# Kernel optimization log

Hardware: AMD Instinct MI355X
Metric: run time of the kernel (lower is better)

## Reference

```python
import jax, jax.numpy as jnp
import numpy as np

N = 65536      # occupied voxels
D = 96         # voxel grid extent per axis
CIN = 64
CH = 64
COUT = 16      # 8 * 2
K = 27         # 3^3 kernel offsets


def _build_neighbor_idx(rng):
    # unique occupied voxel coordinates
    lin = rng.choice(D ** 3, size=N, replace=False).astype(np.int64)
    coords = np.stack(np.unravel_index(lin, (D, D, D)), axis=1)  # [N,3]
    grid = np.full(D ** 3, -1, dtype=np.int32)
    grid[lin] = np.arange(N, dtype=np.int32)
    # 27 offsets in {-1,0,1}^3 (MinkowskiEngine kernel map, stride 1)
    offs = np.stack(np.meshgrid(*([np.arange(-1, 2)] * 3), indexing='ij'),
                    axis=-1).reshape(K, 3)
    nc = coords[:, None, :] + offs[None, :, :]            # [N,27,3]
    valid = np.all((nc >= 0) & (nc < D), axis=-1)         # [N,27]
    nlin = (nc[..., 0] * D + nc[..., 1]) * D + nc[..., 2]
    nidx = np.where(valid, grid[np.clip(nlin, 0, D ** 3 - 1)], -1)
    return nidx.astype(np.int32)                          # -1 = no neighbor


def setup_inputs() -> dict:
    key = jax.random.key(0)
    ks = jax.random.split(key, 7)
    rng = np.random.default_rng(0)
    neighbor_idx = jnp.asarray(_build_neighbor_idx(rng))
    s1 = 1.0 / np.sqrt(K * CIN)
    s2 = 1.0 / np.sqrt(K * CH)
    return {
        'x': jax.random.normal(ks[0], (N, CIN), jnp.float32),
        'neighbor_idx': neighbor_idx,
        'W1': jax.random.normal(ks[1], (K, CIN, CH), jnp.float32) * s1,
        'b1': jax.random.normal(ks[2], (CH,), jnp.float32) * 0.1,
        'W2': jax.random.normal(ks[3], (K, CH, CH), jnp.float32) * s2,
        'b2': jax.random.normal(ks[4], (CH,), jnp.float32) * 0.1,
        'W3': jax.random.normal(ks[5], (K, CH, COUT), jnp.float32) * s2,
        'b3': jax.random.normal(ks[6], (COUT,), jnp.float32) * 0.1,
    }


def _sparse_conv(feat, W, b, nidx):
    # feat: [N,Cin], W: [K,Cin,Cout], nidx: [N,K] with -1 for missing
    mask = nidx >= 0
    gathered = jnp.where(mask[..., None],
                         feat[jnp.clip(nidx, 0)], 0.0)    # [N,K,Cin]
    return jnp.einsum('nkc,kcd->nd', gathered, W) + b


def reference(x, neighbor_idx, W1, b1, W2, b2, W3, b3):
    h = jax.nn.relu(_sparse_conv(x, W1, b1, neighbor_idx))
    h = jax.nn.relu(_sparse_conv(h, W2, b2, neighbor_idx))
    return _sparse_conv(h, W3, b3, neighbor_idx)
```

## Files before the change

### kernel.cpp

```cpp
#include <hip/hip_runtime.h>
#include <hip/hip_bf16.h>
#include <stdint.h>

#define N_VOX 65536
#define NK 27
#define BR 64

typedef float f32x4  __attribute__((ext_vector_type(4)));
typedef float f32x16 __attribute__((ext_vector_type(16)));
typedef int   i32x2  __attribute__((ext_vector_type(2)));
typedef __bf16 bf16x8 __attribute__((ext_vector_type(8)));

#define WAITVM(n) asm volatile("s_waitcnt vmcnt(" #n ")" ::: "memory")

__device__ __forceinline__ void barrier_fence() {
    asm volatile("" ::: "memory");
    __builtin_amdgcn_s_barrier();
    asm volatile("" ::: "memory");
}

__device__ __forceinline__ void gll16(const void* src, uint32_t lds_addr) {
    asm volatile("s_mov_b32 m0, %0\n\t"
                 "global_load_lds_dwordx4 %1, off"
                 :: "s"(lds_addr), "v"(src)
                 : "memory");
}

__device__ __forceinline__ void wconv_elem(const float* __restrict__ W,
                                           __bf16* __restrict__ Wt, int Dc, int i) {
    int d = i % Dc;
    int c = (i / Dc) % 64;
    int k = i / (Dc * 64);
    int off = ((d * 128 + ((c >> 3) << 4)) ^ ((d & 7) << 4)) + (c & 7) * 2;
    *(__bf16*)((char*)Wt + (size_t)k * Dc * 128 + off) = (__bf16)W[i];
}

#define PREP_CVT   2048
#define PREP_W1    432
#define PREP_W2    432
#define PREP_W3    108
#define PREP_GRID  (PREP_CVT + PREP_W1 + PREP_W2 + PREP_W3 + 1)
__global__ __launch_bounds__(256) void prep_kernel(
    const float* __restrict__ x,
    const float* __restrict__ W1, const float* __restrict__ W2, const float* __restrict__ W3,
    __bf16* __restrict__ xb, __bf16* __restrict__ Wt1, __bf16* __restrict__ Wt2,
    __bf16* __restrict__ Wt3, float* __restrict__ zp)
{
    const int b = blockIdx.x, tid = threadIdx.x;
    if (b < PREP_CVT) {
        int i = b * 256 + tid;
        const f32x4* xp = (const f32x4*)x;
        f32x4 f0 = xp[i * 2], f1 = xp[i * 2 + 1];
        bf16x8 v;
#pragma unroll
        for (int j = 0; j < 4; ++j) { v[j] = (__bf16)f0[j]; v[4 + j] = (__bf16)f1[j]; }
        ((bf16x8*)xb)[i] = v;
    } else if (b < PREP_CVT + PREP_W1) {
        wconv_elem(W1, Wt1, 64, (b - PREP_CVT) * 256 + tid);
    } else if (b < PREP_CVT + PREP_W1 + PREP_W2) {
        wconv_elem(W2, Wt2, 64, (b - PREP_CVT - PREP_W1) * 256 + tid);
    } else if (b < PREP_CVT + PREP_W1 + PREP_W2 + PREP_W3) {
        wconv_elem(W3, Wt3, 16, (b - PREP_CVT - PREP_W1 - PREP_W2) * 256 + tid);
    } else {
        if (tid < 16) ((f32x4*)zp)[tid] = (f32x4){0.f, 0.f, 0.f, 0.f};
    }
}

__device__ __forceinline__ int xcd_swz(int b, int nwg) {
    return (b & 7) * (nwg >> 3) + (b >> 3);
}

__global__ __launch_bounds__(256, 4) void conv_ch(
    const __bf16* __restrict__ feat,
    const int* __restrict__ nidx,
    const __bf16* __restrict__ Wt,
    const float* __restrict__ bias,
    __bf16* __restrict__ dst,
    const __bf16* __restrict__ zp)
{
    constexpr int ABSZ = BR * 128;
    constexpr int BSZ  = 64 * 128;
    constexpr int BOFF = 2 * ABSZ;
    constexpr int SNOFF = BOFF + 2 * BSZ;
    __shared__ __align__(16) char lds[SNOFF + BR * NK * 4];

    const int tid = threadIdx.x;
    const int lane = tid & 63;
    const int wid = tid >> 6;
    const int wr = wid >> 1;
    const int wc = wid & 1;
    const int row0 = xcd_swz(blockIdx.x, gridDim.x) * BR;

    int* snid = (int*)(lds + SNOFF);
    const int* gnid = nidx + (size_t)row0 * NK;
    for (int i = tid; i < BR * NK; i += 256) {
        int r = i / NK;
        int kk = i - r * NK;
        snid[kk * 64 + (r & 7) * 8 + (r >> 3)] = gnid[i];
    }
    __syncthreads();

    const uint32_t ldsbase = (uint32_t)(uintptr_t)(&lds[0]);
    const int qA = ((lane & 7) ^ (lane >> 3)) << 4;

    auto issueB = [&](int k, int buf) {
#pragma unroll
        for (int j = 0; j < 2; ++j) {
            int jb = wid * 2 + j;
            gll16(Wt + (size_t)k * 4096 + jb * 512 + lane * 8,
                  (uint32_t)__builtin_amdgcn_readfirstlane(
                      (int)(ldsbase + BOFF + buf * BSZ + jb * 1024)));
        }
    };

    auto issueA = [&](int k, int buf) {
        i32x2 mv = *(const i32x2*)(snid + k * 64 + (lane >> 3) * 8 + wid * 2);
#pragma unroll
        for (int j = 0; j < 2; ++j) {
            int m = mv[j];
            const __bf16* src = (m >= 0)
                ? (const __bf16*)((const char*)feat + (size_t)m * 128 + qA) : zp;
            gll16(src, (uint32_t)__builtin_amdgcn_readfirstlane(
                           (int)(ldsbase + buf * ABSZ + (wid * 2 + j) * 1024)));
        }
    };

    f32x16 acc;
#pragma unroll
    for (int j = 0; j < 16; ++j) acc[j] = 0.f;

    auto compute = [&](int k) {
        const char* Ac = lds + (k & 1) * ABSZ;
        const char* Bc = lds + BOFF + (k & 1) * BSZ;
        const int arow = wr * 32 + (lane & 31);
        const int brow = wc * 32 + (lane & 31);
        const int hi16 = (lane >> 5) << 4;
        bf16x8 a[4], b[4];
#pragma unroll
        for (int s = 0; s < 4; ++s) {
            a[s] = *(const bf16x8*)(Ac + ((arow * 128 + s * 32 + hi16)
                                          ^ ((arow & 7) << 4)));
            b[s] = *(const bf16x8*)(Bc + ((brow * 128 + s * 32 + hi16)
                                          ^ ((brow & 7) << 4)));
        }
#pragma unroll
        for (int s = 0; s < 4; ++s)
            acc = __builtin_amdgcn_mfma_f32_32x32x16_bf16(a[s], b[s], acc, 0, 0, 0);
    };

    issueB(0, 0);
    issueA(0, 0);

    for (int k = 0; k < NK; ++k) {
        const int buf = k & 1;
        barrier_fence();
        if (k + 1 < NK) {
            issueB(k + 1, buf ^ 1);
            issueA(k + 1, buf ^ 1);
            WAITVM(4);
        } else {
            WAITVM(0);
        }
        barrier_fence();
        compute(k);
    }

    const int c = wc * 32 + (lane & 31);
    const float bv = bias[c];
#pragma unroll
    for (int reg = 0; reg < 16; ++reg) {
        int r = row0 + wr * 32 + (reg & 3) + 8 * (reg >> 2) + 4 * (lane >> 5);
        float v = fmaxf(acc[reg] + bv, 0.f);
        dst[(size_t)r * 64 + c] = (__bf16)v;
    }
}

__global__ __launch_bounds__(256, 4) void conv_l3(
    const __bf16* __restrict__ feat, const int* __restrict__ nidx,
    const __bf16* __restrict__ Wt, const float* __restrict__ bias,
    float* __restrict__ dst, const __bf16* __restrict__ zp)
{
    constexpr int ABSZ = 64 * 128;
    constexpr int BSZ = 16 * 128;
    constexpr int BOFF = 2 * ABSZ;
    constexpr int SNOFF = BOFF + 2 * BSZ;
    __shared__ __align__(16) char lds[SNOFF + 64 * NK * 4];

    const int tid = threadIdx.x;
    const int lane = tid & 63;
    const int wid = tid >> 6;
    const int col = lane & 15;
    const int kgrp = lane >> 4;
    const int row0 = xcd_swz(blockIdx.x, gridDim.x) * 64;

    int* snid = (int*)(lds + SNOFF);
    const int* gnid = nidx + (size_t)row0 * NK;
    for (int i = tid; i < 64 * NK; i += 256) {
        int r = i / NK;
        int kk = i - r * NK;
        snid[kk * 64 + (r & 7) * 8 + (r >> 3)] = gnid[i];
    }
    __syncthreads();

    const uint32_t ldsbase = (uint32_t)(uintptr_t)(&lds[0]);
    const int qA = ((lane & 7) ^ (lane >> 3)) << 4;

    auto issueB = [&](int k, int buf) {
        if (wid < 2)
            gll16(Wt + (size_t)k * 1024 + wid * 512 + lane * 8,
                  (uint32_t)__builtin_amdgcn_readfirstlane(
                      (int)(ldsbase + BOFF + buf * BSZ + wid * 1024)));
    };
    auto issueA = [&](int k, int buf) {
        i32x2 mv = *(const i32x2*)(snid + k * 64 + (lane >> 3) * 8 + wid * 2);
#pragma unroll
        for (int j = 0; j < 2; ++j) {
            int m = mv[j];
            const __bf16* src = (m >= 0)
                ? (const __bf16*)((const char*)feat + (size_t)m * 128 + qA) : zp;
            gll16(src, (uint32_t)__builtin_amdgcn_readfirstlane(
                           (int)(ldsbase + buf * ABSZ + (wid * 2 + j) * 1024)));
        }
    };

    f32x4 acc;
#pragma unroll
    for (int j = 0; j < 4; ++j) acc[j] = 0.f;

    auto compute = [&](int k) {
        const char* Ac = lds + (k & 1) * ABSZ;
        const char* Bc = lds + BOFF + (k & 1) * BSZ;
        int ar = wid * 16 + col;
        bf16x8 a[2], b[2];
#pragma unroll
        for (int kk = 0; kk < 2; ++kk) {
            a[kk] = *(const bf16x8*)(Ac + ((ar * 128 + kk * 64 + kgrp * 16)
                                           ^ ((ar & 7) << 4)));
            b[kk] = *(const bf16x8*)(Bc + ((col * 128 + kk * 64 + kgrp * 16)
                                           ^ ((col & 7) << 4)));
        }
#pragma unroll
        for (int kk = 0; kk < 2; ++kk)
            acc = __builtin_amdgcn_mfma_f32_16x16x32_bf16(a[kk], b[kk], acc, 0, 0, 0);
    };

    issueB(0, 0);
    issueA(0, 0);
    for (int k = 0; k < NK; ++k) {
        const int buf = k & 1;
        barrier_fence();
        if (k + 1 < NK) {
            issueB(k + 1, buf ^ 1);
            issueA(k + 1, buf ^ 1);
            if (wid < 2) { WAITVM(3); } else { WAITVM(2); }
        } else {
            WAITVM(0);
        }
        barrier_fence();
        compute(k);
    }

    float bv = bias[col];
#pragma unroll
    for (int reg = 0; reg < 4; ++reg) {
        int r = row0 + wid * 16 + kgrp * 4 + reg;
        dst[(size_t)r * 16 + col] = acc[reg] + bv;
    }
}

extern "C" void kernel_launch(void* const* d_in, const int* in_sizes, int n_in,
                              void* d_out, int out_size, void* d_ws, size_t ws_size,
                              hipStream_t stream) {
    const float* x  = (const float*)d_in[0];
    const int* nidx = (const int*)d_in[1];
    const float* W1 = (const float*)d_in[2];
    const float* b1 = (const float*)d_in[3];
    const float* W2 = (const float*)d_in[4];
    const float* b2 = (const float*)d_in[5];
    const float* W3 = (const float*)d_in[6];
    const float* b3 = (const float*)d_in[7];

    char* ws = (char*)d_ws;
    __bf16* buf0 = (__bf16*)ws;
    __bf16* buf1 = (__bf16*)(ws + 8388608);
    __bf16* Wt1  = (__bf16*)(ws + 16777216);
    __bf16* Wt2  = Wt1 + 27 * 64 * 64;
    __bf16* Wt3  = Wt2 + 27 * 64 * 64;
    __bf16* zp   = Wt3 + 27 * 16 * 64;

    prep_kernel<<<PREP_GRID, 256, 0, stream>>>(x, W1, W2, W3, buf0, Wt1, Wt2, Wt3, (float*)zp);

    conv_ch<<<N_VOX / BR, 256, 0, stream>>>(buf0, nidx, Wt1, b1, buf1, zp);
    conv_ch<<<N_VOX / BR, 256, 0, stream>>>(buf1, nidx, Wt2, b2, buf0, zp);
    conv_l3<<<N_VOX / 64, 256, 0, stream>>>(buf0, nidx, Wt3, b3, (float*)d_out, zp);
}
```

Measured before the change: 73.09 us.

## Triple-buffer conv_ch pipeline, compress neighbor indices, switch to 16x16 MFMA tiles

conv_ch moves from double to triple buffering with a prefetch distance of two and one barrier per iteration instead of two, aiming to hide gather latency better. Neighbor indices are stored in LDS as 16-bit values, with validity kept as per-offset bitmasks built by atomicOr. The MMA tiling changes from one 32x32x16 to four 16x16x32 MFMAs per wave. The XCD block swizzle is removed and occupancy is lowered to 3 blocks per SM to fit the larger LDS footprint. That costs latency hiding and L2 locality across XCDs.

Result: slower. 76.89 us (+5.2%).

```diff
diff --git a/kernel.cpp b/kernel.cpp
--- a/kernel.cpp
+++ b/kernel.cpp
@@ -7,8 +7,8 @@
 #define BR 64
 
 typedef float f32x4  __attribute__((ext_vector_type(4)));
-typedef float f32x16 __attribute__((ext_vector_type(16)));
 typedef int   i32x2  __attribute__((ext_vector_type(2)));
+typedef unsigned short u16x2 __attribute__((ext_vector_type(2)));
 typedef __bf16 bf16x8 __attribute__((ext_vector_type(8)));
 
 #define WAITVM(n) asm volatile("s_waitcnt vmcnt(" #n ")" ::: "memory")
@@ -66,11 +66,7 @@
     }
 }
 
-__device__ __forceinline__ int xcd_swz(int b, int nwg) {
-    return (b & 7) * (nwg >> 3) + (b >> 3);
-}
-
-__global__ __launch_bounds__(256, 4) void conv_ch(
+__global__ __launch_bounds__(256, 3) void conv_ch(
     const __bf16* __restrict__ feat,
     const int* __restrict__ nidx,
     const __bf16* __restrict__ Wt,
@@ -80,98 +76,125 @@
 {
     constexpr int ABSZ = BR * 128;
     constexpr int BSZ  = 64 * 128;
-    constexpr int BOFF = 2 * ABSZ;
-    constexpr int SNOFF = BOFF + 2 * BSZ;
-    __shared__ __align__(16) char lds[SNOFF + BR * NK * 4];
+    constexpr int BOFF = 3 * ABSZ;
+    constexpr int SNOFF = BOFF + 3 * BSZ;
+    constexpr int VMOFF = SNOFF + NK * 64 * 2;
+    __shared__ __align__(16) char lds[VMOFF + NK * 2 * 4 + 40];
 
     const int tid = threadIdx.x;
     const int lane = tid & 63;
     const int wid = tid >> 6;
     const int wr = wid >> 1;
     const int wc = wid & 1;
-    const int row0 = xcd_swz(blockIdx.x, gridDim.x) * BR;
-
-    int* snid = (int*)(lds + SNOFF);
+    const int col = lane & 15;
+    const int kgrp = lane >> 4;
+    const int row0 = blockIdx.x * BR;
+
+    uint16_t* snid = (uint16_t*)(lds + SNOFF);
+    unsigned* vm = (unsigned*)(lds + VMOFF);
+
+    if (tid < NK * 2) vm[tid] = 0u;
+    __syncthreads();
     const int* gnid = nidx + (size_t)row0 * NK;
     for (int i = tid; i < BR * NK; i += 256) {
         int r = i / NK;
         int kk = i - r * NK;
-        snid[kk * 64 + (r & 7) * 8 + (r >> 3)] = gnid[i];
+        int m = gnid[i];
+        snid[kk * 64 + (r & 7) * 8 + (r >> 3)] = (uint16_t)m;
+        if (m >= 0) atomicOr(&vm[kk * 2 + (r >> 5)], 1u << (r & 31));
     }
     __syncthreads();
 
     const uint32_t ldsbase = (uint32_t)(uintptr_t)(&lds[0]);
     const int qA = ((lane & 7) ^ (lane >> 3)) << 4;
-
-    auto issueB = [&](int k, int buf) {
+    const char* featB = (const char*)feat;
+    const char* zpB = (const char*)zp;
+    const int vbit0 = (wid & 1) * 16 + (lane >> 3);
+
+    auto issueK = [&](int k, int wb) {
 #pragma unroll
         for (int j = 0; j < 2; ++j) {
             int jb = wid * 2 + j;
             gll16(Wt + (size_t)k * 4096 + jb * 512 + lane * 8,
                   (uint32_t)__builtin_amdgcn_readfirstlane(
-                      (int)(ldsbase + BOFF + buf * BSZ + jb * 1024)));
-        }
-    };
-
-    auto issueA = [&](int k, int buf) {
-        i32x2 mv = *(const i32x2*)(snid + k * 64 + (lane >> 3) * 8 + wid * 2);
+                      (int)(ldsbase + BOFF + wb * BSZ + jb * 1024)));
+        }
+        u16x2 mv = *(const u16x2*)(snid + k * 64 + (lane >> 3) * 8 + wid * 2);
+        unsigned w = vm[k * 2 + (wid >> 1)];
 #pragma unroll
         for (int j = 0; j < 2; ++j) {
-            int m = mv[j];
-            const __bf16* src = (m >= 0)
-                ? (const __bf16*)((const char*)feat + (size_t)m * 128 + qA) : zp;
+            bool valid = (w >> (vbit0 + j * 8)) & 1u;
+            const char* src = valid ? (featB + (size_t)(unsigned)mv[j] * 128 + qA) : zpB;
             gll16(src, (uint32_t)__builtin_amdgcn_readfirstlane(
-                           (int)(ldsbase + buf * ABSZ + (wid * 2 + j) * 1024)));
-        }
-    };
-
-    f32x16 acc;
-#pragma unroll
-    for (int j = 0; j < 16; ++j) acc[j] = 0.f;
-
-    auto compute = [&](int k) {
-        const char* Ac = lds + (k & 1) * ABSZ;
-        const char* Bc = lds + BOFF + (k & 1) * BSZ;
-        const int arow = wr * 32 + (lane & 31);
-        const int brow = wc * 32 + (lane & 31);
-        const int hi16 = (lane >> 5) << 4;
-        bf16x8 a[4], b[4];
-#pragma unroll
-        for (int s = 0; s < 4; ++s) {
-            a[s] = *(const bf16x8*)(Ac + ((arow * 128 + s * 32 + hi16)
-                                          ^ ((arow & 7) << 4)));
-            b[s] = *(const bf16x8*)(Bc + ((brow * 128 + s * 32 + hi16)
-                                          ^ ((brow & 7) << 4)));
-        }
-#pragma unroll
-        for (int s = 0; s < 4; ++s)
-            acc = __builtin_amdgcn_mfma_f32_32x32x16_bf16(a[s], b[s], acc, 0, 0, 0);
-    };
-
-    issueB(0, 0);
-    issueA(0, 0);
-
+                           (int)(ldsbase + wb * ABSZ + (wid * 2 + j) * 1024)));
+        }
+    };
+
+    f32x4 acc[2][2];
+#pragma unroll
+    for (int mi = 0; mi < 2; ++mi)
+#pragma unroll
+        for (int ni = 0; ni < 2; ++ni)
+#pragma unroll
+            for (int j = 0; j < 4; ++j) acc[mi][ni][j] = 0.f;
+
+    auto compute = [&](int bs) {
+        const char* Ac = lds + bs * ABSZ;
+        const char* Bc = lds + BOFF + bs * BSZ;
+        bf16x8 a[2][2], b[2][2];
+#pragma unroll
+        for (int mi = 0; mi < 2; ++mi) {
+            int ar = wr * 32 + mi * 16 + col;
+#pragma unroll
+            for (int kk = 0; kk < 2; ++kk)
+                a[mi][kk] = *(const bf16x8*)(Ac + ((ar * 128 + kk * 64 + kgrp * 16)
+                                                   ^ ((ar & 7) << 4)));
+        }
+#pragma unroll
+        for (int ni = 0; ni < 2; ++ni) {
+            int br = wc * 32 + ni * 16 + col;
+#pragma unroll
+            for (int kk = 0; kk < 2; ++kk)
+                b[ni][kk] = *(const bf16x8*)(Bc + ((br * 128 + kk * 64 + kgrp * 16)
+                                                   ^ ((br & 7) << 4)));
+        }
+#pragma unroll
+        for (int kk = 0; kk < 2; ++kk)
+#pragma unroll
+            for (int mi = 0; mi < 2; ++mi)
+#pragma unroll
+                for (int ni = 0; ni < 2; ++ni)
+                    acc[mi][ni] = __builtin_amdgcn_mfma_f32_16x16x32_bf16(
+                        a[mi][kk], b[ni][kk], acc[mi][ni], 0, 0, 0);
+    };
+
+    issueK(0, 0);
+    issueK(1, 1);
+
+    int bs = 0, wb = 2;
     for (int k = 0; k < NK; ++k) {
-        const int buf = k & 1;
+        if (k < NK - 1) { WAITVM(4); }
+        else { WAITVM(0); }
         barrier_fence();
-        if (k + 1 < NK) {
-            issueB(k + 1, buf ^ 1);
-            issueA(k + 1, buf ^ 1);
-            WAITVM(4);
-        } else {
-            WAITVM(0);
-        }
-        barrier_fence();
-        compute(k);
-    }
-
-    const int c = wc * 32 + (lane & 31);
-    const float bv = bias[c];
-#pragma unroll
-    for (int reg = 0; reg < 16; ++reg) {
-        int r = row0 + wr * 32 + (reg & 3) + 8 * (reg >> 2) + 4 * (lane >> 5);
-        float v = fmaxf(acc[reg] + bv, 0.f);
-        dst[(size_t)r * 64 + c] = (__bf16)v;
+        if (k + 2 < NK) issueK(k + 2, wb);
+        compute(bs);
+        if (++bs == 3) bs = 0;
+        if (++wb == 3) wb = 0;
+    }
+
+#pragma unroll
+    for (int ni = 0; ni < 2; ++ni) {
+        int c = wc * 32 + ni * 16 + col;
+        float bv = bias[c];
+#pragma unroll
+        for (int mi = 0; mi < 2; ++mi) {
+#pragma unroll
+            for (int reg = 0; reg < 4; ++reg) {
+                int r = row0 + wr * 32 + mi * 16 + kgrp * 4 + reg;
+                float v = fmaxf(acc[mi][ni][reg] + bv, 0.f);
+                dst[(size_t)r * 64 + c] = (__bf16)v;
+            }
+        }
     }
 }
 
@@ -191,7 +214,7 @@
     const int wid = tid >> 6;
     const int col = lane & 15;
     const int kgrp = lane >> 4;
-    const int row0 = xcd_swz(blockIdx.x, gridDim.x) * 64;
+    const int row0 = blockIdx.x * 64;
 
     int* snid = (int*)(lds + SNOFF);
     const int* gnid = nidx + (size_t)row0 * NK;
```
